# Optimization experiments

Hardware: AMD Instinct MI355X
Metric: run time of the kernel (lower is better)

Reference implementation:

```python
import jax, jax.numpy as jnp
from jax import lax
import numpy as np

B, L, D, KSIZE = 8, 2048, 256, 8


def setup_inputs() -> dict:
    key = jax.random.key(0)
    kx, kw, kwin, kb, ktau = jax.random.split(key, 5)
    scale = 1.0 / np.sqrt(D).astype(np.float32)
    x = jax.random.normal(kx, (B, L, D), dtype=jnp.float32)
    weight = jax.random.normal(kw, (D, D), dtype=jnp.float32) * scale
    input_weight = jax.random.normal(kwin, (D, D), dtype=jnp.float32) * scale
    bias = jax.random.normal(kb, (1, D), dtype=jnp.float32)
    # tau = |randn| in the original; offset by 1 to keep 1/tau numerically sane
    tau = jnp.abs(jax.random.normal(ktau, (1, D), dtype=jnp.float32)) + 1.0
    return {"x": x, "weight": weight, "input_weight": input_weight,
            "bias": bias, "tau": tau, "ksize": KSIZE}


def reference(x, weight, input_weight, bias, tau, ksize):
    b, l, d = x.shape
    # get_K: left-pad with (ksize-1) zeros, gather overlapping windows
    xp = jnp.pad(x, ((0, 0), (ksize - 1, 0), (0, 0)))
    idx = jnp.arange(l)[:, None] + jnp.arange(ksize)[None, :]  # (l, ksize)
    windows = xp[:, idx, :]                                    # (b, l, ksize, d)
    xw = windows.reshape(b * l, ksize, d)                      # flatten per-window batch

    inv_tau = 1.0 / tau                                        # (1, d)
    h0 = jnp.zeros((b * l, d), dtype=x.dtype)

    def step(h, xt):
        # SimpleCTRNN update: h += (1/tau) * (-h + relu(h W + x W_in + b))
        h_new = h + inv_tau * (-h + jax.nn.relu(h @ weight + xt @ input_weight + bias))
        return h_new, None

    xs = jnp.swapaxes(xw, 0, 1)                                # (ksize, b*l, d)
    h_last, _ = lax.scan(step, h0, xs)
    # forward() keeps only the last window timestep
    return h_last.reshape(b, l, d)
```

## Files before the change

kernel.cpp:

```cpp
#include <hip/hip_runtime.h>

typedef __bf16 bf16_t;
typedef __bf16 bf16x8 __attribute__((ext_vector_type(8)));
typedef float  f32x4  __attribute__((ext_vector_type(4)));

#define Ldim 2048
#define Ddim 256
#define MROWS 64

__global__ void swz_kernel(const float* __restrict__ w,
                           const float* __restrict__ win,
                           bf16_t* __restrict__ wsw,
                           bf16_t* __restrict__ winsw) {
    int mat = blockIdx.x >> 3, kt = blockIdx.x & 7;
    const float* src = mat ? win : w;
    bf16_t*      dst = mat ? winsw : wsw;
    int ln = threadIdx.x & 63, g = threadIdx.x >> 6;
    int c = ln & 15, q = ln >> 4;
#pragma unroll
    for (int i = 0; i < 4; ++i) {
        int nt = g + 4 * i;
        bf16x8 v;
#pragma unroll
        for (int j = 0; j < 8; ++j)
            v[j] = (bf16_t)src[(kt * 32 + q * 8 + j) * Ddim + nt * 16 + c];
        *(bf16x8*)&dst[((kt * 16 + nt) * 64 + ln) * 8] = v;
    }
}

__global__ __launch_bounds__(256, 1)
void rnn_kernel(const float* __restrict__ x,
                const float* __restrict__ bias,
                const float* __restrict__ tau,
                const bf16x8* __restrict__ wsw,
                const bf16x8* __restrict__ winsw,
                float* __restrict__ out)
{
    __shared__ bf16_t hbuf[4 * 8 * 512];
    char* hb = (char*)hbuf;

    const int tid = threadIdx.x;
    const int w   = tid >> 6;
    const int ln  = tid & 63;
    const int c   = ln & 15;
    const int q   = ln >> 4;
    const int blk = blockIdx.x;
    const int bb  = blk >> 5;
    const int l0  = (blk & 31) * MROWS;

    int   ncol[4];
    float itau[4];
#pragma unroll
    for (int nl = 0; nl < 4; ++nl) {
        ncol[nl] = (4 * w + nl) * 16 + c;
        itau[nl] = 1.0f / tau[ncol[nl]];
    }

    f32x4 au[5][4];
#pragma unroll
    for (int nl = 0; nl < 4; ++nl) {
        float bv = bias[ncol[nl]];
#pragma unroll
        for (int mt = 0; mt < 5; ++mt) {
            f32x4 t = {bv, bv, bv, bv};
            au[mt][nl] = t;
        }
    }

    const float* xb = x + (long)bb * (Ldim * Ddim);
    const f32x4 zf = {0.f, 0.f, 0.f, 0.f};

    auto loadX = [&](f32x4 (&buf)[5][2], int kt) {
#pragma unroll
        for (int mt = 0; mt < 5; ++mt) {
            int  lrow = l0 - 7 + mt * 16 + c;
            bool ok   = (lrow >= 0) && (lrow < Ldim);
            const f32x4* p = (const f32x4*)(xb + (long)lrow * Ddim + kt * 32 + q * 8);
            buf[mt][0] = ok ? p[0] : zf;
            buf[mt][1] = ok ? p[1] : zf;
        }
    };
    auto loadW = [&](bf16x8 (&wb)[4], int kt) {
#pragma unroll
        for (int nl = 0; nl < 4; ++nl)
            wb[nl] = winsw[(kt * 16 + 4 * w + nl) * 64 + ln];
    };
    auto step1 = [&](const f32x4 (&buf)[5][2], const bf16x8 (&wb)[4]) {
        bf16x8 aF[5];
#pragma unroll
        for (int mt = 0; mt < 5; ++mt)
#pragma unroll
            for (int jj = 0; jj < 4; ++jj) {
                aF[mt][jj]     = (bf16_t)buf[mt][0][jj];
                aF[mt][jj + 4] = (bf16_t)buf[mt][1][jj];
            }
#pragma unroll
        for (int nl = 0; nl < 4; ++nl)
#pragma unroll
            for (int mt = 0; mt < 5; ++mt)
                au[mt][nl] = __builtin_amdgcn_mfma_f32_16x16x32_bf16(
                    aF[mt], wb[nl], au[mt][nl], 0, 0, 0);
    };

    {
        f32x4  x0[5][2], x1[5][2];
        bf16x8 w0[4], w1[4];
        loadX(x0, 0); loadW(w0, 0);
#pragma unroll 1
        for (int kk = 0; kk < 4; ++kk) {
            loadX(x1, 2 * kk + 1); loadW(w1, 2 * kk + 1);
            step1(x0, w0);
            if (kk < 3) { loadX(x0, 2 * kk + 2); loadW(w0, 2 * kk + 2); }
            step1(x1, w1);
        }
    }

    bf16x8 bfr[8][4];
#pragma unroll
    for (int kt = 0; kt < 8; ++kt)
#pragma unroll
        for (int nl = 0; nl < 4; ++nl)
            bfr[kt][nl] = wsw[(kt * 16 + 4 * w + nl) * 64 + ln];

    int offn[4];
#pragma unroll
    for (int nl = 0; nl < 4; ++nl) {
        int kk = ncol[nl];
        offn[nl] = (kk >> 5) * 1024 + ((kk >> 3) & 3) * 64 + q * 16 + (kk & 7) * 2;
    }
    const int permln = (((ln & 3) << 4) | ((ln >> 4) << 2) | ((ln >> 2) & 3)) * 16;
    const int sl     = (ln + 16) & 63;

    f32x4 h[4][4];
#pragma unroll
    for (int mt = 0; mt < 4; ++mt)
#pragma unroll
        for (int nl = 0; nl < 4; ++nl)
#pragma unroll
            for (int r = 0; r < 4; ++r)
                h[mt][nl][r] = itau[nl] * fmaxf(au[mt][nl][r], 0.0f);

#pragma unroll 1
    for (int t = 1; t < 8; ++t) {
#pragma unroll
        for (int nl = 0; nl < 4; ++nl) {
            float a[5];
#pragma unroll
            for (int mt = 0; mt < 5; ++mt) a[mt] = __shfl(au[mt][nl][0], sl);
#pragma unroll
            for (int mt = 0; mt < 5; ++mt) {
                float n3 = (q < 3) ? a[mt] : (mt < 4 ? a[mt + 1] : a[mt]);
                f32x4 o = au[mt][nl];
                f32x4 s = {o[1], o[2], o[3], n3};
                au[mt][nl] = s;
            }
        }
#pragma unroll
        for (int mt = 0; mt < 4; ++mt)
#pragma unroll
            for (int nl = 0; nl < 4; ++nl)
#pragma unroll
                for (int r = 0; r < 4; ++r)
                    *(bf16_t*)(hb + mt * 8192 + r * 256 + offn[nl]) =
                        (bf16_t)h[mt][nl][r];
        __syncthreads();
        f32x4 acc[4][4];
#pragma unroll
        for (int kt = 0; kt < 8; ++kt) {
            bf16x8 aF[4];
#pragma unroll
            for (int mt = 0; mt < 4; ++mt)
                aF[mt] = *(const bf16x8*)(hb + (mt * 8 + kt) * 1024 + permln);
#pragma unroll
            for (int nl = 0; nl < 4; ++nl)
#pragma unroll
                for (int mt = 0; mt < 4; ++mt)
                    acc[mt][nl] = __builtin_amdgcn_mfma_f32_16x16x32_bf16(
                        aF[mt], bfr[kt][nl],
                        (kt == 0) ? au[mt][nl] : acc[mt][nl], 0, 0, 0);
        }
        __syncthreads();
#pragma unroll
        for (int mt = 0; mt < 4; ++mt)
#pragma unroll
            for (int nl = 0; nl < 4; ++nl)
#pragma unroll
                for (int r = 0; r < 4; ++r) {
                    float hh = h[mt][nl][r];
                    float s  = fmaxf(acc[mt][nl][r], 0.0f);
                    h[mt][nl][r] = hh + itau[nl] * (s - hh);
                }
    }

    float* ob = out + ((long)bb * Ldim + l0) * Ddim;
#pragma unroll
    for (int mt = 0; mt < 4; ++mt)
#pragma unroll
        for (int nl = 0; nl < 4; ++nl)
#pragma unroll
            for (int r = 0; r < 4; ++r)
                ob[(mt * 16 + 4 * q + r) * Ddim + ncol[nl]] = h[mt][nl][r];
}

extern "C" void kernel_launch(void* const* d_in, const int* in_sizes, int n_in,
                              void* d_out, int out_size, void* d_ws, size_t ws_size,
                              hipStream_t stream) {
    const float* x            = (const float*)d_in[0];
    const float* weight       = (const float*)d_in[1];
    const float* input_weight = (const float*)d_in[2];
    const float* bias         = (const float*)d_in[3];
    const float* tau          = (const float*)d_in[4];
    (void)in_sizes; (void)n_in; (void)out_size; (void)ws_size;

    bf16_t* wsw   = (bf16_t*)d_ws;
    bf16_t* winsw = wsw + 65536;

    swz_kernel<<<16, 256, 0, stream>>>(weight, input_weight, wsw, winsw);
    rnn_kernel<<<256, 256, 0, stream>>>(x, bias, tau,
                                        (const bf16x8*)wsw, (const bf16x8*)winsw,
                                        (float*)d_out);
}
```

Baseline: 108.0 us.

## Fuse weight swizzle into RNN kernel and double-buffer LDS hidden state

Drops the separate weight-swizzle kernel launch: each block now reads fp32 W and W_in straight from global memory and converts them to bf16 MFMA fragments in registers, overlapping the W loads with the input-projection MFMAs. The hidden-state LDS buffer is double-buffered so the second barrier per timestep can go. LDS writes pack bf16 pairs across neighbouring lanes with DPP to issue 32-bit stores. In exchange, every block does strided fp32 weight loads and conversions itself, which adds global traffic and register pressure.

```diff
diff --git a/kernel.cpp b/kernel.cpp
--- a/kernel.cpp
+++ b/kernel.cpp
@@ -8,36 +8,22 @@
 #define Ddim 256
 #define MROWS 64
 
-__global__ void swz_kernel(const float* __restrict__ w,
-                           const float* __restrict__ win,
-                           bf16_t* __restrict__ wsw,
-                           bf16_t* __restrict__ winsw) {
-    int mat = blockIdx.x >> 3, kt = blockIdx.x & 7;
-    const float* src = mat ? win : w;
-    bf16_t*      dst = mat ? winsw : wsw;
-    int ln = threadIdx.x & 63, g = threadIdx.x >> 6;
-    int c = ln & 15, q = ln >> 4;
-#pragma unroll
-    for (int i = 0; i < 4; ++i) {
-        int nt = g + 4 * i;
-        bf16x8 v;
-#pragma unroll
-        for (int j = 0; j < 8; ++j)
-            v[j] = (bf16_t)src[(kt * 32 + q * 8 + j) * Ddim + nt * 16 + c];
-        *(bf16x8*)&dst[((kt * 16 + nt) * 64 + ln) * 8] = v;
-    }
+__device__ inline unsigned int bfbits(float f) {
+    bf16_t b = (bf16_t)f;
+    unsigned short u;
+    __builtin_memcpy(&u, &b, 2);
+    return (unsigned int)u;
 }
 
 __global__ __launch_bounds__(256, 1)
 void rnn_kernel(const float* __restrict__ x,
+                const float* __restrict__ wgt,
+                const float* __restrict__ win,
                 const float* __restrict__ bias,
                 const float* __restrict__ tau,
-                const bf16x8* __restrict__ wsw,
-                const bf16x8* __restrict__ winsw,
                 float* __restrict__ out)
 {
-    __shared__ bf16_t hbuf[4 * 8 * 512];
-    char* hb = (char*)hbuf;
+    __shared__ char hb[2 * 32768];
 
     const int tid = threadIdx.x;
     const int w   = tid >> 6;
@@ -80,10 +66,15 @@
             buf[mt][1] = ok ? p[1] : zf;
         }
     };
-    auto loadW = [&](bf16x8 (&wb)[4], int kt) {
-#pragma unroll
-        for (int nl = 0; nl < 4; ++nl)
-            wb[nl] = winsw[(kt * 16 + 4 * w + nl) * 64 + ln];
+    auto loadWF = [&](bf16x8 (&wb)[4], const float* __restrict__ src, int kt) {
+        const float* base = src + (long)(kt * 32 + q * 8) * Ddim + c;
+#pragma unroll
+        for (int nl = 0; nl < 4; ++nl) {
+            const float* p = base + (4 * w + nl) * 16;
+#pragma unroll
+            for (int j = 0; j < 8; ++j)
+                wb[nl][j] = (bf16_t)p[(long)j * Ddim];
+        }
     };
     auto step1 = [&](const f32x4 (&buf)[5][2], const bf16x8 (&wb)[4]) {
         bf16x8 aF[5];
@@ -102,32 +93,29 @@
                     aF[mt], wb[nl], au[mt][nl], 0, 0, 0);
     };
 
+    bf16x8 bfr[8][4];
     {
         f32x4  x0[5][2], x1[5][2];
         bf16x8 w0[4], w1[4];
-        loadX(x0, 0); loadW(w0, 0);
-#pragma unroll 1
+        loadX(x0, 0); loadWF(w0, win, 0);
+#pragma unroll
         for (int kk = 0; kk < 4; ++kk) {
-            loadX(x1, 2 * kk + 1); loadW(w1, 2 * kk + 1);
+            loadX(x1, 2 * kk + 1); loadWF(w1, win, 2 * kk + 1);
+            loadWF(bfr[2 * kk], wgt, 2 * kk);
             step1(x0, w0);
-            if (kk < 3) { loadX(x0, 2 * kk + 2); loadW(w0, 2 * kk + 2); }
+            if (kk < 3) { loadX(x0, 2 * kk + 2); loadWF(w0, win, 2 * kk + 2); }
+            loadWF(bfr[2 * kk + 1], wgt, 2 * kk + 1);
             step1(x1, w1);
         }
     }
 
-    bf16x8 bfr[8][4];
-#pragma unroll
-    for (int kt = 0; kt < 8; ++kt)
-#pragma unroll
-        for (int nl = 0; nl < 4; ++nl)
-            bfr[kt][nl] = wsw[(kt * 16 + 4 * w + nl) * 64 + ln];
-
-    int offn[4];
+    int offnp[4];
 #pragma unroll
     for (int nl = 0; nl < 4; ++nl) {
-        int kk = ncol[nl];
-        offn[nl] = (kk >> 5) * 1024 + ((kk >> 3) & 3) * 64 + q * 16 + (kk & 7) * 2;
-    }
+        int kk2 = ncol[nl] & ~1;
+        offnp[nl] = (kk2 >> 5) * 1024 + ((kk2 >> 3) & 3) * 64 + q * 16 + (kk2 & 7) * 2;
+    }
+    const int codd   = c & 1;
     const int permln = (((ln & 3) << 4) | ((ln >> 4) << 2) | ((ln >> 2) & 3)) * 16;
     const int sl     = (ln + 16) & 63;
 
@@ -142,6 +130,7 @@
 
 #pragma unroll 1
     for (int t = 1; t < 8; ++t) {
+        char* hbw = hb + ((t - 1) & 1) * 32768;
 #pragma unroll
         for (int nl = 0; nl < 4; ++nl) {
             float a[5];
@@ -158,11 +147,21 @@
 #pragma unroll
         for (int mt = 0; mt < 4; ++mt)
 #pragma unroll
-            for (int nl = 0; nl < 4; ++nl)
-#pragma unroll
-                for (int r = 0; r < 4; ++r)
-                    *(bf16_t*)(hb + mt * 8192 + r * 256 + offn[nl]) =
-                        (bf16_t)h[mt][nl][r];
+            for (int nl = 0; nl < 4; ++nl) {
+                unsigned int P[4];
+#pragma unroll
+                for (int r = 0; r < 4; ++r) {
+                    unsigned int own = bfbits(h[mt][nl][r]);
+                    unsigned int par = (unsigned int)__builtin_amdgcn_mov_dpp(
+                        (int)own, 0xB1, 0xF, 0xF, true);
+                    P[r] = codd ? (par | (own << 16)) : (own | (par << 16));
+                }
+                unsigned int v0 = codd ? P[1] : P[0];
+                unsigned int v1 = codd ? P[3] : P[2];
+                char* bp = hbw + mt * 8192 + codd * 256 + offnp[nl];
+                *(unsigned int*)bp         = v0;
+                *(unsigned int*)(bp + 512) = v1;
+            }
         __syncthreads();
         f32x4 acc[4][4];
 #pragma unroll
@@ -170,7 +169,7 @@
             bf16x8 aF[4];
 #pragma unroll
             for (int mt = 0; mt < 4; ++mt)
-                aF[mt] = *(const bf16x8*)(hb + (mt * 8 + kt) * 1024 + permln);
+                aF[mt] = *(const bf16x8*)(hbw + (mt * 8 + kt) * 1024 + permln);
 #pragma unroll
             for (int nl = 0; nl < 4; ++nl)
 #pragma unroll
@@ -179,7 +178,6 @@
                         aF[mt], bfr[kt][nl],
                         (kt == 0) ? au[mt][nl] : acc[mt][nl], 0, 0, 0);
         }
-        __syncthreads();
 #pragma unroll
         for (int mt = 0; mt < 4; ++mt)
 #pragma unroll
@@ -210,13 +208,8 @@
     const float* input_weight = (const float*)d_in[2];
     const float* bias         = (const float*)d_in[3];
     const float* tau          = (const float*)d_in[4];
-    (void)in_sizes; (void)n_in; (void)out_size; (void)ws_size;
-
-    bf16_t* wsw   = (bf16_t*)d_ws;
-    bf16_t* winsw = wsw + 65536;
-
-    swz_kernel<<<16, 256, 0, stream>>>(weight, input_weight, wsw, winsw);
-    rnn_kernel<<<256, 256, 0, stream>>>(x, bias, tau,
-                                        (const bf16x8*)wsw, (const bf16x8*)winsw,
+    (void)in_sizes; (void)n_in; (void)out_size; (void)d_ws; (void)ws_size;
+
+    rnn_kernel<<<256, 256, 0, stream>>>(x, weight, input_weight, bias, tau,
                                         (float*)d_out);
 }
```

Result: no change. 109.9 us (+1.8%).
